# Performance work log

Hardware: AMD Instinct MI355X
Metric: run time of the kernel (lower is better)

## Reference

```python
import jax, jax.numpy as jnp
import numpy as np

D_MODEL = 1024

def _positional_encoding(seq_len: int, d_model: int) -> jnp.ndarray:
    # value = pos / 10000 ** (2*dim/d_model); sin on even dims, cos on odd dims
    pos = jnp.arange(seq_len, dtype=jnp.float32)[:, None]          # [S,1]
    dim = jnp.arange(d_model, dtype=jnp.float32)[None, :]          # [1,D]
    val = pos / jnp.power(jnp.float32(10000.0), 2.0 * dim / d_model)
    even = (jnp.arange(d_model) % 2) == 0
    return jnp.where(even[None, :], jnp.sin(val), jnp.cos(val))    # [S,D]

def setup_inputs() -> dict:
    key = jax.random.key(0)
    x = jax.random.normal(key, (8, 4096, D_MODEL), dtype=jnp.float32)
    return {"input": x}

def reference(input) -> jnp.ndarray:
    seq_len, d_model = input.shape[1], input.shape[2]
    pe = _positional_encoding(seq_len, d_model)                    # [S,D]
    return input + pe[None, :, :]                                  # broadcast over batch
```

## Files before the change

### kernel.cpp

```cpp
#include <hip/hip_runtime.h>
#include <hip/hip_bf16.h>
#include <math.h>


#define PE_D 1024
#define PE_S 4096
#define PE_B 8

__global__ __launch_bounds__(256) void
PositionalEncoderModule_48455821033878_kernel(const float* __restrict__ x,
                                              float* __restrict__ out) {
    const int tid = blockIdx.x * blockDim.x + threadIdx.x;
    const int d4  = tid & (PE_D / 4 - 1);
    const int s   = (tid >> 8) & (PE_S - 1);
    const int d0  = d4 << 2;

    const size_t base = (size_t)tid * 4;
    const float4 v = *(const float4*)(x + base);

    const float pos = (float)s;
    const float c = -0.025952563241307517f;

    float4 pe;
    pe.x = sinf(pos * exp2f(c * (float)(d0 + 0)));
    pe.y = cosf(pos * exp2f(c * (float)(d0 + 1)));
    pe.z = sinf(pos * exp2f(c * (float)(d0 + 2)));
    pe.w = cosf(pos * exp2f(c * (float)(d0 + 3)));

    float4 r;
    r.x = v.x + pe.x;
    r.y = v.y + pe.y;
    r.z = v.z + pe.z;
    r.w = v.w + pe.w;
    *(float4*)(out + base) = r;
}

extern "C" void kernel_launch(void* const* d_in, const int* in_sizes, int n_in,
                              void* d_out, int out_size, void* d_ws, size_t ws_size,
                              hipStream_t stream) {
    const float* x = (const float*)d_in[0];
    float* out     = (float*)d_out;

    const int n_threads = PE_B * PE_S * PE_D / 4;
    const int block = 256;
    const int grid  = n_threads / block;

    PositionalEncoderModule_48455821033878_kernel<<<grid, block, 0, stream>>>(x, out);
}
```

Measured before the change: 220.5 us.

## Precompute positional-encoding table once per call and broadcast-add from workspace

Splits the kernel into an init kernel that computes the S×D sin/cos table into the workspace once, followed by an add kernel that reads x and the table. This cuts transcendental work by the batch factor, since the old kernel recomputed the encoding for every batch element. In exchange it adds a second launch, a 16MB table write, and table reads that mostly hit cache. The fused path remains as a fallback when the workspace is too small.

```diff
diff --git a/kernel.cpp b/kernel.cpp
--- a/kernel.cpp
+++ b/kernel.cpp
@@ -8,8 +8,43 @@
 #define PE_B 8
 
 __global__ __launch_bounds__(256) void
-PositionalEncoderModule_48455821033878_kernel(const float* __restrict__ x,
-                                              float* __restrict__ out) {
+pe_init_kernel(float* __restrict__ pe) {
+    const int tid = blockIdx.x * blockDim.x + threadIdx.x;
+    const int d4  = tid & (PE_D / 4 - 1);
+    const int s   = tid >> 8;
+    const int d0  = d4 << 2;
+
+    const float pos = (float)s;
+    const float c = -0.025952563241307517f;
+
+    float4 v;
+    v.x = sinf(pos * exp2f(c * (float)(d0 + 0)));
+    v.y = cosf(pos * exp2f(c * (float)(d0 + 1)));
+    v.z = sinf(pos * exp2f(c * (float)(d0 + 2)));
+    v.w = cosf(pos * exp2f(c * (float)(d0 + 3)));
+
+    *(float4*)(pe + (size_t)tid * 4) = v;
+}
+
+__global__ __launch_bounds__(256) void
+pe_add_kernel(const float* __restrict__ x, const float* __restrict__ pe,
+              float* __restrict__ out) {
+    const int tid = blockIdx.x * blockDim.x + threadIdx.x;
+    const int pidx = tid & (PE_S * PE_D / 4 - 1);
+
+    const float4 v = *(const float4*)(x + (size_t)tid * 4);
+    const float4 p = *(const float4*)(pe + (size_t)pidx * 4);
+
+    float4 r;
+    r.x = v.x + p.x;
+    r.y = v.y + p.y;
+    r.z = v.z + p.z;
+    r.w = v.w + p.w;
+    *(float4*)(out + (size_t)tid * 4) = r;
+}
+
+__global__ __launch_bounds__(256) void
+pe_fused_kernel(const float* __restrict__ x, float* __restrict__ out) {
     const int tid = blockIdx.x * blockDim.x + threadIdx.x;
     const int d4  = tid & (PE_D / 4 - 1);
     const int s   = (tid >> 8) & (PE_S - 1);
@@ -41,9 +76,16 @@
     const float* x = (const float*)d_in[0];
     float* out     = (float*)d_out;
 
-    const int n_threads = PE_B * PE_S * PE_D / 4;
-    const int block = 256;
-    const int grid  = n_threads / block;
+    const size_t pe_bytes = (size_t)PE_S * PE_D * sizeof(float);
 
-    PositionalEncoderModule_48455821033878_kernel<<<grid, block, 0, stream>>>(x, out);
+    if (ws_size >= pe_bytes) {
+        float* pe = (float*)d_ws;
+        const int nA = PE_S * PE_D / 4;
+        pe_init_kernel<<<nA / 256, 256, 0, stream>>>(pe);
+        const int nB = PE_B * PE_S * PE_D / 4;
+        pe_add_kernel<<<nB / 256, 256, 0, stream>>>(x, pe, out);
+    } else {
+        const int n = PE_B * PE_S * PE_D / 4;
+        pe_fused_kernel<<<n / 256, 256, 0, stream>>>(x, out);
+    }
 }
```

After: 228.6 us. 3.7% more time.
